# Kernel tuning notes

Hardware: AMD Instinct MI355X
Metric: run time of the kernel (lower is better)

The kernel has to match this reference:

```python
import jax, jax.numpy as jnp
import numpy as np

COMMIT_W = 0.25
ENT_W = 0.1
ENT_T = 0.01
EPS = 1e-5


def setup_inputs() -> dict:
    key = jax.random.key(0)
    kx, kc = jax.random.split(key)
    x = jax.random.normal(kx, (32, 32, 32, 256), dtype=jnp.float32)
    # variance_scaling(1.0, fan_in, uniform) -> U(-sqrt(3/fan_in), sqrt(3/fan_in)), fan_in = 256
    lim = float(np.sqrt(3.0 / 256.0))
    codebook = jax.random.uniform(kc, (1024, 256), dtype=jnp.float32, minval=-lim, maxval=lim)
    return {"x": x, "codebook": codebook}


def _cdist(flat, codebook):
    # Euclidean distance (with sqrt, as jnp.linalg.norm in the original),
    # computed via the expanded quadratic form to avoid the [N,K,D] intermediate.
    d2 = (jnp.sum(flat * flat, axis=-1, keepdims=True)
          + jnp.sum(codebook * codebook, axis=-1)[None, :]
          - 2.0 * (flat @ codebook.T))
    return jnp.sqrt(jnp.maximum(d2, 0.0))  # [N, K]


def reference(x, codebook):
    D = x.shape[-1]
    flat = x.reshape(-1, D)                      # [N, D]
    distances = _cdist(flat, codebook)           # [N, K]
    flat_indices = jnp.argmin(distances, axis=-1)  # [N]
    indices = flat_indices.reshape(x.shape[:-1])
    # one_hot(indices) @ codebook == gather
    quantized = codebook[flat_indices].reshape(x.shape)

    # optax.l2_loss = 0.5 * (pred - target)^2
    commit_loss = 0.5 * jnp.mean((x - jax.lax.stop_gradient(quantized)) ** 2) * COMMIT_W
    codebook_loss = 0.5 * jnp.mean((jax.lax.stop_gradient(x) - quantized) ** 2)

    # entropy loss on affinity = -distances
    logits = (-distances) / ENT_T                # [N, K]
    probs = jax.nn.softmax(logits, axis=-1)
    log_probs = jax.nn.log_softmax(logits + EPS, axis=-1)
    avg_probs = jnp.mean(probs, axis=0)          # [K]
    avg_entropy = -jnp.sum(avg_probs * jnp.log(avg_probs + EPS))
    sample_entropy = -jnp.mean(jnp.sum(probs * log_probs, axis=-1))
    entropy_loss = (sample_entropy - avg_entropy) * ENT_W

    vq_loss = codebook_loss + commit_loss + entropy_loss
    # straight-through estimator
    quantized_st = x + jax.lax.stop_gradient(quantized - x)
    return quantized_st, vq_loss, commit_loss, codebook_loss, entropy_loss, indices
```

## Files before the change

kernel.cpp:

```cpp
#include <hip/hip_runtime.h>

#define N_ROWS 32768
#define DIMS 256
#define K_CODES 1024
#define MT 64
#define NCHUNK 256
#define KC 32
#define SA 68
#define SB 260

static constexpr size_t SC_OFF  = 8388608;
static constexpr size_t IDX_OFF = 8388612;

__device__ inline float wsum64(float v){
  #pragma unroll
  for(int off=32; off; off>>=1) v += __shfl_xor(v, off, 64);
  return v;
}

__global__ __launch_bounds__(256) void rowsq_np512_kernel(const float* __restrict__ X,
                                                          const float* __restrict__ CB,
                                                          float* __restrict__ xsq,
                                                          float* __restrict__ csq){
  const int t = threadIdx.x;
  const int wv = t >> 6, l = t & 63;
  const int sub = l >> 4, li = l & 15;
  #pragma unroll
  for(int p=0; p<4; p++){
    int r = blockIdx.x*64 + p*16 + wv*4 + sub;
    const float* s0; float* dst;
    if(r < K_CODES){ s0 = CB + (size_t)r*DIMS; dst = csq + r; }
    else { s0 = X + (size_t)(r - K_CODES)*DIMS; dst = xsq + (r - K_CODES); }
    float blk[2];
    #pragma unroll
    for(int bb=0; bb<2; bb++){
      float q[8];
      #pragma unroll
      for(int j=0;j<8;j++){
        float a = s0[bb*128 + j*16 + li];
        q[j] = __fmul_rn(a, a);
      }
      float v = __fadd_rn(__fadd_rn(__fadd_rn(q[0],q[1]), __fadd_rn(q[2],q[3])),
                          __fadd_rn(__fadd_rn(q[4],q[5]), __fadd_rn(q[6],q[7])));
      v = __fadd_rn(v, __shfl_xor(v, 8, 64));
      v = __fadd_rn(v, __shfl_xor(v, 4, 64));
      v = __fadd_rn(v, __shfl_xor(v, 2, 64));
      v = __fadd_rn(v, __shfl_xor(v, 1, 64));
      blk[bb] = v;
    }
    if(li == 0) *dst = __fadd_rn(blk[0], blk[1]);
  }
}

__global__ __launch_bounds__(256,2) void fused_argmin_kernel(
    const float* __restrict__ X, const float* __restrict__ CB,
    const float* __restrict__ xsq, const float* __restrict__ csq,
    float* __restrict__ hist, float* __restrict__ acc_sc,
    float* __restrict__ out)
{
  __shared__ __align__(16) float As[KC][SA];
  __shared__ __align__(16) float Bs[KC][SB];
  __shared__ __align__(16) float cs_lds[K_CODES];
  __shared__ __align__(16) float xs_lds[MT];
  __shared__ int sk[MT];
  const int t  = threadIdx.x;
  const int tx = t & 31, ty = t >> 5;
  const int m0 = blockIdx.x * MT;

  reinterpret_cast<float4*>(cs_lds)[t] = reinterpret_cast<const float4*>(csq)[t];
  if(t < 16)
    reinterpret_cast<float4*>(xs_lds)[t] = reinterpret_cast<const float4*>(xsq + m0)[t];

  const int arow = t >> 2;
  const int acol = (t & 3) * 8;
  const float* Ag = X + (size_t)(m0 + arow)*DIMS + acol;

  float4 a4p[2], b4p[8];
  #pragma unroll
  for(int q=0;q<2;q++) a4p[q] = *(const float4*)(Ag + q*4);
  {
    const float* Bg = CB + (size_t)t*DIMS;
    #pragma unroll
    for(int q=0;q<8;q++) b4p[q] = *(const float4*)(Bg + q*4);
  }
  __syncthreads();

  float xs_[8];
  { float4 x0 = *(const float4*)&xs_lds[ty*8];
    float4 x1 = *(const float4*)&xs_lds[ty*8+4];
    xs_[0]=x0.x; xs_[1]=x0.y; xs_[2]=x0.z; xs_[3]=x0.w;
    xs_[4]=x1.x; xs_[5]=x1.y; xs_[6]=x1.z; xs_[7]=x1.w; }

  float dm[8]; int km[8]; float Ss[8], Ts[8];

  for(int nc=0; nc<4; nc++){
    const int n0c = nc*NCHUNK;
    float acc[8][8];
    #pragma unroll
    for(int i=0;i<8;i++)
      #pragma unroll
      for(int j=0;j<8;j++) acc[i][j]=0.f;

    for(int kc=0;kc<8;kc++){
      __syncthreads();
      #pragma unroll
      for(int q=0;q<2;q++){
        As[acol+q*4+0][arow]=a4p[q].x; As[acol+q*4+1][arow]=a4p[q].y;
        As[acol+q*4+2][arow]=a4p[q].z; As[acol+q*4+3][arow]=a4p[q].w;
      }
      #pragma unroll
      for(int q=0;q<8;q++){
        Bs[q*4+0][t]=b4p[q].x; Bs[q*4+1][t]=b4p[q].y;
        Bs[q*4+2][t]=b4p[q].z; Bs[q*4+3][t]=b4p[q].w;
      }
      __syncthreads();
      {
        int nkc = kc+1, nnc = nc;
        if(nkc==8){ nkc=0; nnc=(nc+1)&3; }
        const float* An = Ag + nkc*KC;
        const float* Bn = CB + (size_t)(nnc*NCHUNK + t)*DIMS + nkc*KC;
        #pragma unroll
        for(int q=0;q<2;q++) a4p[q]=*(const float4*)(An + q*4);
        #pragma unroll
        for(int q=0;q<8;q++) b4p[q]=*(const float4*)(Bn + q*4);
      }
      #pragma unroll
      for(int k=0;k<KC;k++){
        float4 a0 = *(const float4*)&As[k][ty*8];
        float4 a1 = *(const float4*)&As[k][ty*8+4];
        float4 b0 = *(const float4*)&Bs[k][tx*4];
        float4 b1 = *(const float4*)&Bs[k][128 + tx*4];
        float a_[8]={a0.x,a0.y,a0.z,a0.w, a1.x,a1.y,a1.z,a1.w};
        float b_[8]={b0.x,b0.y,b0.z,b0.w, b1.x,b1.y,b1.z,b1.w};
        #pragma unroll
        for(int r=0;r<8;r++)
          #pragma unroll
          for(int j=0;j<8;j++)
            acc[r][j] = fmaf(a_[r], b_[j], acc[r][j]);
      }
    }

    float csv[8];
    { float4 c0 = *(const float4*)&cs_lds[n0c + tx*4];
      float4 c1 = *(const float4*)&cs_lds[n0c + 128 + tx*4];
      csv[0]=c0.x; csv[1]=c0.y; csv[2]=c0.z; csv[3]=c0.w;
      csv[4]=c1.x; csv[5]=c1.y; csv[6]=c1.z; csv[7]=c1.w; }
    #pragma unroll
    for(int i=0;i<8;i++){
      float xs = xs_[i];
      float d[8];
      #pragma unroll
      for(int j=0;j<8;j++){
        float d2 = (xs + csv[j]) - 2.0f*acc[i][j];
        d[j] = sqrtf(fmaxf(d2, 0.f));
      }
      float dl = INFINITY; int kl = 0;
      #pragma unroll
      for(int j=0;j<8;j++){
        int kidx = n0c + (j>>2)*128 + tx*4 + (j&3);
        if(d[j] < dl){ dl = d[j]; kl = kidx; }
      }
      #pragma unroll
      for(int off=1; off<32; off<<=1){
        float od = __shfl_xor(dl, off, 64);
        int   ok = __shfl_xor(kl, off, 64);
        if(od < dl || (od == dl && ok < kl)){ dl = od; kl = ok; }
      }
      float s1=0.f, t2s=0.f;
      #pragma unroll
      for(int j=0;j<8;j++){
        float l = (dl - d[j])*100.0f;
        float e = expf(l);
        s1 += e; t2s = fmaf(e, l, t2s);
      }
      #pragma unroll
      for(int off=1; off<32; off<<=1){
        s1  += __shfl_xor(s1,  off, 64);
        t2s += __shfl_xor(t2s, off, 64);
      }
      if(nc == 0){
        dm[i]=dl; km[i]=kl; Ss[i]=s1; Ts[i]=t2s;
      } else {
        if(dl < dm[i]){
          float del = 100.0f*(dl - dm[i]); float al = expf(del);
          Ts[i] = al*(Ts[i] + Ss[i]*del) + t2s;
          Ss[i] = al*Ss[i] + s1;
          dm[i] = dl; km[i] = kl;
        } else {
          float del = 100.0f*(dm[i] - dl); float al = expf(del);
          Ts[i] += al*(t2s + s1*del);
          Ss[i] += al*s1;
        }
      }
    }
  }

  float plogp = 0.f;
  if(tx == 0){
    #pragma unroll
    for(int i=0;i<8;i++){
      int n = m0 + ty*8 + i;
      out[IDX_OFF + n] = (float)km[i];
      sk[ty*8 + i] = km[i];
      atomicAdd(hist + km[i], 1.0f);
      plogp += Ts[i]/Ss[i] - logf(Ss[i]);
    }
  }
  plogp = wsum64(plogp);
  if((t & 63) == 0) atomicAdd(acc_sc + 1, plogp);

  __syncthreads();
  {
    int w = t>>6, lane = t&63;
    int row0 = w*16;
    float mse = 0.f;
    for(int r=0;r<16;r++){
      int n = m0 + row0 + r;
      int k = sk[row0 + r];
      float4 cb4 = *(const float4*)(CB + (size_t)k*DIMS + lane*4);
      float4 x4  = *(const float4*)(X  + (size_t)n*DIMS + lane*4);
      float e0=x4.x-cb4.x, e1=x4.y-cb4.y, e2=x4.z-cb4.z, e3=x4.w-cb4.w;
      mse += e0*e0 + e1*e1 + e2*e2 + e3*e3;
      *reinterpret_cast<float4*>(out + (size_t)n*DIMS + lane*4) = cb4;
    }
    mse = wsum64(mse);
    if(lane==0) atomicAdd(acc_sc+0, mse);
  }
}

__global__ __launch_bounds__(256) void finalize_kernel(const float* __restrict__ hist,
                                                       const float* __restrict__ acc_sc,
                                                       float* __restrict__ out){
  __shared__ float red[256];
  int t = threadIdx.x;
  float s = 0.f;
  #pragma unroll
  for(int c=0;c<4;c++){
    float ap = hist[c*256 + t] * (1.0f/32768.0f);
    s += ap * logf(ap + 1e-5f);
  }
  red[t] = s; __syncthreads();
  for(int off=128; off; off>>=1){
    if(t<off) red[t]+=red[t+off];
    __syncthreads();
  }
  if(t==0){
    float avg_entropy    = -red[0];
    float mse            = acc_sc[0] * (1.0f/8388608.0f);
    float sample_entropy = -(acc_sc[1] * (1.0f/32768.0f));
    float commit = 0.5f*mse*0.25f;
    float cbl    = 0.5f*mse;
    float ent    = (sample_entropy - avg_entropy)*0.1f;
    float vq     = cbl + commit + ent;
    out[SC_OFF+0] = vq;
    out[SC_OFF+1] = commit;
    out[SC_OFF+2] = cbl;
    out[SC_OFF+3] = ent;
  }
}

extern "C" void kernel_launch(void* const* d_in, const int* in_sizes, int n_in,
                              void* d_out, int out_size, void* d_ws, size_t ws_size,
                              hipStream_t stream){
  const float* X  = (const float*)d_in[0];
  const float* CB = (const float*)d_in[1];
  float* out = (float*)d_out;
  float* xsq     = (float*)d_ws;
  float* csq     = xsq + N_ROWS;
  float* hist    = csq + K_CODES;
  float* acc_sc  = hist + K_CODES;

  hipMemsetAsync(hist, 0, (K_CODES+2)*sizeof(float), stream);
  rowsq_np512_kernel <<<(K_CODES+N_ROWS)/64, 256, 0, stream>>>(X, CB, xsq, csq);
  fused_argmin_kernel<<<N_ROWS/MT, 256, 0, stream>>>(X, CB, xsq, csq, hist, acc_sc, out);
  finalize_kernel    <<<1, 256, 0, stream>>>(hist, acc_sc, out);
}
```

Baseline: 427.8 us.

## Halve K-chunk depth and move per-chunk softmax stats to shared memory

Halves the depth of each staged reduction chunk from 32 to 16, which halves the A/B prefetch registers and the shared tile size and doubles the number of chunk iterations and barriers. The running per-row argmin and softmax state (dm, km, Ss, Ts) is no longer kept in registers across codebook chunks. Each chunk instead writes its stats to a shared cstat array, and the first 64 threads merge them at the end. The goal is lower register and LDS pressure, allowing higher occupancy, at the cost of more synchronisation per output tile.

```diff
diff --git a/kernel.cpp b/kernel.cpp
--- a/kernel.cpp
+++ b/kernel.cpp
@@ -5,7 +5,7 @@
 #define K_CODES 1024
 #define MT 64
 #define NCHUNK 256
-#define KC 32
+#define KC 16
 #define SA 68
 #define SB 260
 
@@ -62,6 +62,7 @@
   __shared__ __align__(16) float Bs[KC][SB];
   __shared__ __align__(16) float cs_lds[K_CODES];
   __shared__ __align__(16) float xs_lds[MT];
+  __shared__ __align__(16) float4 cstat[4][MT];
   __shared__ int sk[MT];
   const int t  = threadIdx.x;
   const int tx = t & 31, ty = t >> 5;
@@ -72,16 +73,15 @@
     reinterpret_cast<float4*>(xs_lds)[t] = reinterpret_cast<const float4*>(xsq + m0)[t];
 
   const int arow = t >> 2;
-  const int acol = (t & 3) * 8;
+  const int acol = (t & 3) * 4;
   const float* Ag = X + (size_t)(m0 + arow)*DIMS + acol;
 
-  float4 a4p[2], b4p[8];
-  #pragma unroll
-  for(int q=0;q<2;q++) a4p[q] = *(const float4*)(Ag + q*4);
+  float4 a4p, b4p[4];
+  a4p = *(const float4*)(Ag);
   {
     const float* Bg = CB + (size_t)t*DIMS;
     #pragma unroll
-    for(int q=0;q<8;q++) b4p[q] = *(const float4*)(Bg + q*4);
+    for(int q=0;q<4;q++) b4p[q] = *(const float4*)(Bg + q*4);
   }
   __syncthreads();
 
@@ -91,8 +91,6 @@
     xs_[0]=x0.x; xs_[1]=x0.y; xs_[2]=x0.z; xs_[3]=x0.w;
     xs_[4]=x1.x; xs_[5]=x1.y; xs_[6]=x1.z; xs_[7]=x1.w; }
 
-  float dm[8]; int km[8]; float Ss[8], Ts[8];
-
   for(int nc=0; nc<4; nc++){
     const int n0c = nc*NCHUNK;
     float acc[8][8];
@@ -101,28 +99,24 @@
       #pragma unroll
       for(int j=0;j<8;j++) acc[i][j]=0.f;
 
-    for(int kc=0;kc<8;kc++){
+    for(int kc=0;kc<16;kc++){
       __syncthreads();
-      #pragma unroll
-      for(int q=0;q<2;q++){
-        As[acol+q*4+0][arow]=a4p[q].x; As[acol+q*4+1][arow]=a4p[q].y;
-        As[acol+q*4+2][arow]=a4p[q].z; As[acol+q*4+3][arow]=a4p[q].w;
-      }
-      #pragma unroll
-      for(int q=0;q<8;q++){
+      As[acol+0][arow]=a4p.x; As[acol+1][arow]=a4p.y;
+      As[acol+2][arow]=a4p.z; As[acol+3][arow]=a4p.w;
+      #pragma unroll
+      for(int q=0;q<4;q++){
         Bs[q*4+0][t]=b4p[q].x; Bs[q*4+1][t]=b4p[q].y;
         Bs[q*4+2][t]=b4p[q].z; Bs[q*4+3][t]=b4p[q].w;
       }
       __syncthreads();
       {
         int nkc = kc+1, nnc = nc;
-        if(nkc==8){ nkc=0; nnc=(nc+1)&3; }
+        if(nkc==16){ nkc=0; nnc=(nc+1)&3; }
         const float* An = Ag + nkc*KC;
         const float* Bn = CB + (size_t)(nnc*NCHUNK + t)*DIMS + nkc*KC;
+        a4p = *(const float4*)(An);
         #pragma unroll
-        for(int q=0;q<2;q++) a4p[q]=*(const float4*)(An + q*4);
-        #pragma unroll
-        for(int q=0;q<8;q++) b4p[q]=*(const float4*)(Bn + q*4);
+        for(int q=0;q<4;q++) b4p[q]=*(const float4*)(Bn + q*4);
       }
       #pragma unroll
       for(int k=0;k<KC;k++){
@@ -178,33 +172,38 @@
         s1  += __shfl_xor(s1,  off, 64);
         t2s += __shfl_xor(t2s, off, 64);
       }
-      if(nc == 0){
-        dm[i]=dl; km[i]=kl; Ss[i]=s1; Ts[i]=t2s;
+      if(tx == 0)
+        cstat[nc][ty*8 + i] = make_float4(dl, __int_as_float(kl), s1, t2s);
+    }
+  }
+
+  __syncthreads();
+  float plogp = 0.f;
+  if(t < MT){
+    float4 c0 = cstat[0][t];
+    float dm = c0.x; int km = __float_as_int(c0.y);
+    float Ss = c0.z; float Ts = c0.w;
+    #pragma unroll
+    for(int nc=1; nc<4; nc++){
+      float4 cn = cstat[nc][t];
+      float dl = cn.x; int kl = __float_as_int(cn.y);
+      float s1 = cn.z, t2s = cn.w;
+      if(dl < dm){
+        float del = 100.0f*(dl - dm); float al = expf(del);
+        Ts = al*(Ts + Ss*del) + t2s;
+        Ss = al*Ss + s1;
+        dm = dl; km = kl;
       } else {
-        if(dl < dm[i]){
-          float del = 100.0f*(dl - dm[i]); float al = expf(del);
-          Ts[i] = al*(Ts[i] + Ss[i]*del) + t2s;
-          Ss[i] = al*Ss[i] + s1;
-          dm[i] = dl; km[i] = kl;
-        } else {
-          float del = 100.0f*(dm[i] - dl); float al = expf(del);
-          Ts[i] += al*(t2s + s1*del);
-          Ss[i] += al*s1;
-        }
-      }
-    }
-  }
-
-  float plogp = 0.f;
-  if(tx == 0){
-    #pragma unroll
-    for(int i=0;i<8;i++){
-      int n = m0 + ty*8 + i;
-      out[IDX_OFF + n] = (float)km[i];
-      sk[ty*8 + i] = km[i];
-      atomicAdd(hist + km[i], 1.0f);
-      plogp += Ts[i]/Ss[i] - logf(Ss[i]);
-    }
+        float del = 100.0f*(dm - dl); float al = expf(del);
+        Ts += al*(t2s + s1*del);
+        Ss += al*s1;
+      }
+    }
+    int n = m0 + t;
+    out[IDX_OFF + n] = (float)km;
+    sk[t] = km;
+    atomicAdd(hist + km, 1.0f);
+    plogp = Ts/Ss - logf(Ss);
   }
   plogp = wsum64(plogp);
   if((t & 63) == 0) atomicAdd(acc_sc + 1, plogp);
```

Measured after the change: 367.1 us. 1.17x faster.
